# Kernel optimization log

Measured on AMD Instinct MI355X. Metric: run time of the kernel, lower is better.

Reference implementation:

```python
import jax, jax.numpy as jnp
import numpy as np

B, S, D, H = 2, 2048, 1024, 16
HD = D // H


def setup_inputs() -> dict:
    key = jax.random.key(0)
    ks = jax.random.split(key, 6)
    std = 1.0 / np.sqrt(D)
    return {
        "hidden_states": jax.random.normal(ks[0], (B, S, D), dtype=jnp.float32),
        "attention_mask": jnp.zeros((B, 1, S, S), dtype=jnp.float32),
        "Wq": jax.random.normal(ks[1], (D, D), dtype=jnp.float32) * std,
        "bq": jnp.zeros((D,), dtype=jnp.float32),
        "Wk": jax.random.normal(ks[2], (D, D), dtype=jnp.float32) * std,
        "bk": jnp.zeros((D,), dtype=jnp.float32),
        "Wv": jax.random.normal(ks[3], (D, D), dtype=jnp.float32) * std,
        "bv": jnp.zeros((D,), dtype=jnp.float32),
        "Wo": jax.random.normal(ks[4], (D, D), dtype=jnp.float32) * std,
        "bo": jnp.zeros((D,), dtype=jnp.float32),
    }


def reference(hidden_states, attention_mask, Wq, bq, Wk, bk, Wv, bv, Wo, bo):
    scale = HD ** (-0.5)
    # torch Linear: y = x @ W^T + b
    def proj(x, W, b):
        y = jnp.einsum('bsd,ed->bse', x, W) + b
        return y.reshape(B, S, H, HD).transpose(0, 2, 1, 3)  # [B,H,S,HD]
    q = proj(hidden_states, Wq, bq)
    k = proj(hidden_states, Wk, bk)
    v = proj(hidden_states, Wv, bv)
    scores = jnp.einsum('bhqd,bhkd->bhqk', q, k) * scale + attention_mask
    attn = jax.nn.softmax(scores, axis=-1)  # dropout p=0.0 -> identity
    out = jnp.einsum('bhqk,bhkd->bhqd', attn, v)
    out = out.transpose(0, 2, 1, 3).reshape(B, S, D)
    return jnp.einsum('bsd,ed->bse', out, Wo) + bo
```

## Files before the change

kernel.cpp:

```cpp
#include <hip/hip_runtime.h>
#include <hip/hip_bf16.h>
#include <stdint.h>

#define Bb 2
#define Ss 2048
#define Dd 1024
#define Hh 16
#define HD 64

typedef __attribute__((ext_vector_type(8))) __bf16 bf16x8;
typedef __attribute__((ext_vector_type(4))) __bf16 bf16x4;
typedef __attribute__((ext_vector_type(2))) __bf16 bf16x2;
typedef __attribute__((ext_vector_type(4))) float f32x4;
typedef __attribute__((ext_vector_type(16))) float f32x16;

#define LOG2E 1.44269504088896f
#define SCL2 (0.125f * LOG2E)

#define HS_N   (Bb * Ss * Dd)
#define W_N    (Dd * Dd)
#define B_N    (Dd)
#define CAN_HS 0
#define CAN_WQ (CAN_HS + HS_N)
#define CAN_BQ (CAN_WQ + W_N)
#define CAN_WK (CAN_BQ + B_N)
#define CAN_BK (CAN_WK + W_N)
#define CAN_WV (CAN_BK + B_N)
#define CAN_BV (CAN_WV + W_N)
#define CAN_WO (CAN_BV + B_N)
#define CAN_BO (CAN_WO + W_N)
#define CAN_END (CAN_BO + B_N)
#define TSZ    (Bb * Hh * Ss * HD)
#define WS_ELEMS (CAN_END + 4 * TSZ)
#define WS_NEED ((size_t)WS_ELEMS * 2)

__device__ __forceinline__ void gl_lds16(const __bf16* g, __bf16* l) {
  __builtin_amdgcn_global_load_lds(
      (const __attribute__((address_space(1))) void*)g,
      (__attribute__((address_space(3))) void*)l,
      16, 0, 0);
}

__device__ __forceinline__ void cfence() { asm volatile("" ::: "memory"); }

__global__ void canon_kernel(const float* hs, const float* Wq, const float* bq,
                             const float* Wk, const float* bk, const float* Wv,
                             const float* bv, const float* Wo, const float* bo,
                             __bf16* __restrict__ dst) {
  const float* srcs[9] = {hs, Wq, bq, Wk, bk, Wv, bv, Wo, bo};
  const long starts[10] = {CAN_HS, CAN_WQ, CAN_BQ, CAN_WK, CAN_BK,
                           CAN_WV, CAN_BV, CAN_WO, CAN_BO, CAN_END};
  const long nchunks = CAN_END / 8;
  for (long c = blockIdx.x * blockDim.x + threadIdx.x; c < nchunks;
       c += (long)gridDim.x * blockDim.x) {
    const long i = c * 8;
    int seg = 0;
#pragma unroll
    for (int t = 1; t < 9; t++) seg += (i >= starts[t]) ? 1 : 0;
    const float* s = srcs[seg] + (i - starts[seg]);
    bf16x8 v;
#pragma unroll
    for (int e = 0; e < 8; e++) v[e] = (__bf16)s[e];
    *(bf16x8*)(dst + i) = v;
  }
}

template <int MODE, typename OutT>
__global__ __launch_bounds__(256, 2) void gemm_bt(
    const __bf16* __restrict__ A,
    const __bf16* __restrict__ W0, const __bf16* __restrict__ W1,
    const __bf16* __restrict__ W2,
    const __bf16* __restrict__ b0, const __bf16* __restrict__ b1,
    const __bf16* __restrict__ b2,
    OutT* __restrict__ O0, OutT* __restrict__ O1, OutT* __restrict__ O2) {
  __shared__ __align__(16) __bf16 sA[128 * 32];
  __shared__ __align__(16) __bf16 sB[128 * 32];
  const int tid = threadIdx.x;
  const int lane = tid & 63;
  const int wid = tid >> 6;
  const int quad = lane >> 4;
  const int l15 = lane & 15;
  const int mBlock = blockIdx.x * 128;

  const __bf16* W;
  const __bf16* bias;
  OutT* Out;
  int nBlock, which = 0;
  if (MODE == 0) {
    which = blockIdx.y >> 3;
    nBlock = (blockIdx.y & 7) * 128;
    W = which == 0 ? W0 : (which == 1 ? W1 : W2);
    bias = which == 0 ? b0 : (which == 1 ? b1 : b2);
    Out = which == 0 ? O0 : (which == 1 ? O1 : O2);
  } else {
    nBlock = blockIdx.y * 128;
    W = W0;
    bias = b0;
    Out = O0;
  }

  const int waveM = (wid >> 1) * 64;
  const int waveN = (wid & 1) * 64;

  f32x4 acc[4][4] = {};

  const int c1 = wid * 64 + lane;
  const int c2 = c1 + 256;
  const __bf16* Ar1 = A + (mBlock + (c1 >> 2)) * Dd + (c1 & 3) * 8;
  const __bf16* Ar2 = A + (mBlock + (c2 >> 2)) * Dd + (c2 & 3) * 8;
  const __bf16* Wr1 = W + (nBlock + (c1 >> 2)) * Dd + (c1 & 3) * 8;
  const __bf16* Wr2 = W + (nBlock + (c2 >> 2)) * Dd + (c2 & 3) * 8;
  __bf16* ldsA1 = sA + (wid * 64) * 8;
  __bf16* ldsA2 = sA + (wid * 64 + 256) * 8;
  __bf16* ldsB1 = sB + (wid * 64) * 8;
  __bf16* ldsB2 = sB + (wid * 64 + 256) * 8;

  for (int k0 = 0; k0 < Dd; k0 += 32) {
    gl_lds16(Ar1 + k0, ldsA1);
    gl_lds16(Ar2 + k0, ldsA2);
    gl_lds16(Wr1 + k0, ldsB1);
    gl_lds16(Wr2 + k0, ldsB2);
    __syncthreads();

    bf16x8 aF[4], bF[4];
#pragma unroll
    for (int mi = 0; mi < 4; mi++)
      aF[mi] = *(const bf16x8*)(sA + (waveM + mi * 16 + l15) * 32 + quad * 8);
#pragma unroll
    for (int ni = 0; ni < 4; ni++)
      bF[ni] = *(const bf16x8*)(sB + (waveN + ni * 16 + l15) * 32 + quad * 8);
#pragma unroll
    for (int mi = 0; mi < 4; mi++)
#pragma unroll
      for (int ni = 0; ni < 4; ni++)
        acc[mi][ni] = __builtin_amdgcn_mfma_f32_16x16x32_bf16(
            aF[mi], bF[ni], acc[mi][ni], 0, 0, 0);
    __syncthreads();
  }

#pragma unroll
  for (int ni = 0; ni < 4; ni++) {
    const int ng = nBlock + waveN + ni * 16 + l15;
    const float bv = (float)bias[ng];
#pragma unroll
    for (int mi = 0; mi < 4; mi++) {
      const int mg0 = mBlock + waveM + mi * 16 + quad * 4;
      if (MODE == 0 && which == 2) {
        const int b = mg0 >> 11, s0 = mg0 & 2047;
        const int h = ng >> 6, hd = ng & 63;
        bf16x4 pk;
#pragma unroll
        for (int r = 0; r < 4; r++) pk[r] = (__bf16)(acc[mi][ni][r] + bv);
        *(bf16x4*)((__bf16*)Out + (((b * Hh + h) * HD + hd) * Ss) + s0) = pk;
      } else {
#pragma unroll
        for (int r = 0; r < 4; r++) {
          float v = acc[mi][ni][r] + bv;
          const int m = mg0 + r;
          if (MODE == 0) {
            if (which == 0) v *= SCL2;
            const int b = m >> 11, s = m & 2047;
            const int h = ng >> 6, hd = ng & 63;
            Out[(((b * Hh + h) * Ss + s) * HD) + hd] = (OutT)v;
          } else {
            Out[m * Dd + ng] = (OutT)v;
          }
        }
      }
    }
  }
}

__global__ __launch_bounds__(256, 4) void attn_fused(
    const __bf16* __restrict__ Qg, const __bf16* __restrict__ Kg,
    const __bf16* __restrict__ Vt, const float* __restrict__ Mf,
    __bf16* __restrict__ Og) {
  __shared__ __align__(16) union {
    __bf16 buf[2][8192];
    struct {
      float O[2][64][32];
      float L[2][32];
    } m;
  } sh;

  const int tid = threadIdx.x;
  const int lane = tid & 63;
  const int wid = tid >> 6;
  const int qg = wid & 1;
  const int kvh = wid >> 1;
  const int l31 = lane & 31;
  const int hi = lane >> 5;
  const int bh = blockIdx.y;
  const int b = bh >> 4;
  const int h = bh & 15;
  const int qw = blockIdx.x * 64 + qg * 32 + l31;

  const __bf16* Qp = Qg + (size_t)bh * Ss * HD;
  const __bf16* Kp = Kg + (size_t)bh * Ss * HD;
  const __bf16* Vp = Vt + (size_t)bh * HD * Ss;
  const float* Mrow = Mf + ((size_t)b * Ss + qw) * Ss + 32 * kvh + 4 * hi;

  bf16x8 qf[4];
#pragma unroll
  for (int k = 0; k < 4; k++)
    qf[k] = *(const bf16x8*)(Qp + (size_t)qw * HD + k * 16 + hi * 8);

  const int cA = tid, cB = 256 + tid;
#define STAGE_KV(BI, KVS)                                                     \
  {                                                                           \
    __bf16* kb = sh.buf[BI];                                                  \
    gl_lds16(Kp + ((KVS) + ((cA & 255) >> 2)) * HD + (cA >> 8) * 32 +         \
                 (cA & 3) * 8, kb + cA * 8);                                  \
    gl_lds16(Kp + ((KVS) + ((cB & 255) >> 2)) * HD + (cB >> 8) * 32 +         \
                 (cB & 3) * 8, kb + cB * 8);                                  \
    __bf16* vb = sh.buf[BI] + 4096;                                           \
    gl_lds16(Vp + (size_t)((cA & 255) >> 2) * Ss + (KVS) + (cA >> 8) * 32 +   \
                 (cA & 3) * 8, vb + cA * 8);                                  \
    gl_lds16(Vp + (size_t)((cB & 255) >> 2) * Ss + (KVS) + (cB >> 8) * 32 +   \
                 (cB & 3) * 8, vb + cB * 8);                                  \
  }

  f32x16 o[2] = {};
  f32x4 lacc = {0.f, 0.f, 0.f, 0.f};

  STAGE_KV(0, 0);

  for (int it = 0; it < 32; ++it) {
    const int kv0 = it * 64;
    const int bufc = it & 1;
    cfence();
    __builtin_amdgcn_s_barrier();
    cfence();
    f32x4 mc[4];
#pragma unroll
    for (int g = 0; g < 4; g++) mc[g] = *(const f32x4*)(Mrow + kv0 + g * 8);
    cfence();
    if (it < 31) {
      STAGE_KV(bufc ^ 1, kv0 + 64);
      cfence();
      asm volatile("s_waitcnt vmcnt(8)" ::: "memory");
    } else {
      asm volatile("s_waitcnt vmcnt(4)" ::: "memory");
    }
    __builtin_amdgcn_s_barrier();
    cfence();

    f32x16 sacc = {};
#pragma unroll
    for (int k = 0; k < 4; k++) {
      bf16x8 kf = *(const bf16x8*)(sh.buf[bufc] +
                                   ((k >> 1) * 64 + kvh * 32 + l31) * 32 +
                                   (k & 1) * 16 + hi * 8);
      sacc = __builtin_amdgcn_mfma_f32_32x32x16_bf16(kf, qf[k], sacc, 0, 0, 0);
    }

    f32x4 sv[4];
#pragma unroll
    for (int g = 0; g < 4; g++)
#pragma unroll
      for (int r = 0; r < 4; r++)
        sv[g][r] = __builtin_amdgcn_exp2f(sacc[g * 4 + r] + mc[g][r] * LOG2E);
    lacc += (sv[0] + sv[1]) + (sv[2] + sv[3]);

    bf16x4 pk[4];
#pragma unroll
    for (int g = 0; g < 4; g++)
#pragma unroll
      for (int r = 0; r < 4; r++) pk[g][r] = (__bf16)sv[g][r];
    union pu { bf16x4 v; uint32_t w[2]; };
    pu s0, s1, r0, r1;
    s0.v = hi ? pk[0] : pk[1];
    s1.v = hi ? pk[2] : pk[3];
    r0.w[0] = __shfl_xor((int)s0.w[0], 32);
    r0.w[1] = __shfl_xor((int)s0.w[1], 32);
    r1.w[0] = __shfl_xor((int)s1.w[0], 32);
    r1.w[1] = __shfl_xor((int)s1.w[1], 32);
    bf16x8 pf[2];
    {
      bf16x4 lo0 = hi ? r0.v : pk[0], hi0 = hi ? pk[1] : r0.v;
      bf16x4 lo1 = hi ? r1.v : pk[2], hi1 = hi ? pk[3] : r1.v;
#pragma unroll
      for (int e = 0; e < 4; e++) {
        pf[0][e] = lo0[e]; pf[0][e + 4] = hi0[e];
        pf[1][e] = lo1[e]; pf[1][e + 4] = hi1[e];
      }
    }

#pragma unroll
    for (int k = 0; k < 2; k++)
#pragma unroll
      for (int hb = 0; hb < 2; hb++) {
        bf16x8 vf = *(const bf16x8*)(sh.buf[bufc] + 4096 +
                                     (kvh * 64 + hb * 32 + l31) * 32 +
                                     k * 16 + hi * 8);
        o[hb] = __builtin_amdgcn_mfma_f32_32x32x16_bf16(vf, pf[k], o[hb],
                                                        0, 0, 0);
      }
  }

  float l = lacc[0] + lacc[1] + lacc[2] + lacc[3];
  l += __shfl_xor(l, 32);

  __syncthreads();
  if (kvh == 1) {
#pragma unroll
    for (int hb = 0; hb < 2; hb++)
#pragma unroll
      for (int r = 0; r < 16; r++) {
        const int hd = hb * 32 + (r & 3) + 8 * (r >> 2) + 4 * hi;
        sh.m.O[qg][hd][l31] = o[hb][r];
      }
    if (hi == 0) sh.m.L[qg][l31] = l;
  }
  __syncthreads();
  if (kvh == 0) {
#pragma unroll
    for (int hb = 0; hb < 2; hb++)
#pragma unroll
      for (int r = 0; r < 16; r++) {
        const int hd = hb * 32 + (r & 3) + 8 * (r >> 2) + 4 * hi;
        o[hb][r] += sh.m.O[qg][hd][l31];
      }
    l += sh.m.L[qg][l31];
    const float inv = 1.0f / l;
    __bf16* Ow = Og + (((size_t)b * Ss + qw) * Hh + h) * HD;
#pragma unroll
    for (int hb = 0; hb < 2; hb++)
#pragma unroll
      for (int g = 0; g < 4; g++) {
        const int hd = hb * 32 + g * 8 + 4 * hi;
        bf16x2 w0, w1;
        w0[0] = (__bf16)(o[hb][g * 4 + 0] * inv);
        w0[1] = (__bf16)(o[hb][g * 4 + 1] * inv);
        w1[0] = (__bf16)(o[hb][g * 4 + 2] * inv);
        w1[1] = (__bf16)(o[hb][g * 4 + 3] * inv);
        *(bf16x2*)(Ow + hd) = w0;
        *(bf16x2*)(Ow + hd + 2) = w1;
      }
  }
}

extern "C" void kernel_launch(void* const* d_in, const int* in_sizes, int n_in,
                              void* d_out, int out_size, void* d_ws,
                              size_t ws_size, hipStream_t stream) {
  if (ws_size < WS_NEED) return;

  __bf16* ws = (__bf16*)d_ws;
  const __bf16* hsC = ws + CAN_HS;
  const __bf16* WqC = ws + CAN_WQ;
  const __bf16* bqC = ws + CAN_BQ;
  const __bf16* WkC = ws + CAN_WK;
  const __bf16* bkC = ws + CAN_BK;
  const __bf16* WvC = ws + CAN_WV;
  const __bf16* bvC = ws + CAN_BV;
  const __bf16* WoC = ws + CAN_WO;
  const __bf16* boC = ws + CAN_BO;
  __bf16* Q = ws + CAN_END;
  __bf16* K = Q + TSZ;
  __bf16* V = K + TSZ;
  __bf16* AW = V + TSZ;
  float* out = (float*)d_out;

  canon_kernel<<<2048, 256, 0, stream>>>(
      (const float*)d_in[0], (const float*)d_in[2], (const float*)d_in[3],
      (const float*)d_in[4], (const float*)d_in[5], (const float*)d_in[6],
      (const float*)d_in[7], (const float*)d_in[8], (const float*)d_in[9], ws);
  gemm_bt<0, __bf16><<<dim3(32, 24), 256, 0, stream>>>(
      hsC, WqC, WkC, WvC, bqC, bkC, bvC, Q, K, V);
  attn_fused<<<dim3(32, 32), 256, 0, stream>>>(Q, K, V, (const float*)d_in[1],
                                               AW);
  gemm_bt<1, float><<<dim3(32, 8), 256, 0, stream>>>(
      AW, WoC, WoC, WoC, boC, boC, boC, out, out, out);
}
```

Before: 256.0 us.

## Split output GEMM into narrower-tile kernel and relayout attention K/V LDS tiles

The templated GEMM is split into a QKV-projection kernel and a dedicated output-projection kernel. The output kernel uses 128x64 tiles with K-step 64, which doubles the grid to 512 blocks for better CU coverage and halves barrier count per K. Separately, the attention kernel's K/V shared-memory staging is relaid out into 16-element-wide sub-tiles, with matching fragment read addresses, likely to reduce LDS bank conflicts. The trade-off is more redundant A-tile loads in the output GEMM and more duplicated code.

```diff
diff --git a/kernel.cpp b/kernel.cpp
--- a/kernel.cpp
+++ b/kernel.cpp
@@ -65,14 +65,13 @@
   }
 }
 
-template <int MODE, typename OutT>
-__global__ __launch_bounds__(256, 2) void gemm_bt(
+__global__ __launch_bounds__(256, 2) void gemm_qkv(
     const __bf16* __restrict__ A,
     const __bf16* __restrict__ W0, const __bf16* __restrict__ W1,
     const __bf16* __restrict__ W2,
     const __bf16* __restrict__ b0, const __bf16* __restrict__ b1,
     const __bf16* __restrict__ b2,
-    OutT* __restrict__ O0, OutT* __restrict__ O1, OutT* __restrict__ O2) {
+    __bf16* __restrict__ O0, __bf16* __restrict__ O1, __bf16* __restrict__ O2) {
   __shared__ __align__(16) __bf16 sA[128 * 32];
   __shared__ __align__(16) __bf16 sB[128 * 32];
   const int tid = threadIdx.x;
@@ -82,22 +81,11 @@
   const int l15 = lane & 15;
   const int mBlock = blockIdx.x * 128;
 
-  const __bf16* W;
-  const __bf16* bias;
-  OutT* Out;
-  int nBlock, which = 0;
-  if (MODE == 0) {
-    which = blockIdx.y >> 3;
-    nBlock = (blockIdx.y & 7) * 128;
-    W = which == 0 ? W0 : (which == 1 ? W1 : W2);
-    bias = which == 0 ? b0 : (which == 1 ? b1 : b2);
-    Out = which == 0 ? O0 : (which == 1 ? O1 : O2);
-  } else {
-    nBlock = blockIdx.y * 128;
-    W = W0;
-    bias = b0;
-    Out = O0;
-  }
+  const int which = blockIdx.y >> 3;
+  const int nBlock = (blockIdx.y & 7) * 128;
+  const __bf16* W = which == 0 ? W0 : (which == 1 ? W1 : W2);
+  const __bf16* bias = which == 0 ? b0 : (which == 1 ? b1 : b2);
+  __bf16* Out = which == 0 ? O0 : (which == 1 ? O1 : O2);
 
   const int waveM = (wid >> 1) * 64;
   const int waveN = (wid & 1) * 64;
@@ -110,10 +98,10 @@
   const __bf16* Ar2 = A + (mBlock + (c2 >> 2)) * Dd + (c2 & 3) * 8;
   const __bf16* Wr1 = W + (nBlock + (c1 >> 2)) * Dd + (c1 & 3) * 8;
   const __bf16* Wr2 = W + (nBlock + (c2 >> 2)) * Dd + (c2 & 3) * 8;
-  __bf16* ldsA1 = sA + (wid * 64) * 8;
-  __bf16* ldsA2 = sA + (wid * 64 + 256) * 8;
-  __bf16* ldsB1 = sB + (wid * 64) * 8;
-  __bf16* ldsB2 = sB + (wid * 64 + 256) * 8;
+  __bf16* ldsA1 = sA + c1 * 8;
+  __bf16* ldsA2 = sA + c2 * 8;
+  __bf16* ldsB1 = sB + c1 * 8;
+  __bf16* ldsB2 = sB + c2 * 8;
 
   for (int k0 = 0; k0 < Dd; k0 += 32) {
     gl_lds16(Ar1 + k0, ldsA1);
@@ -145,28 +133,92 @@
 #pragma unroll
     for (int mi = 0; mi < 4; mi++) {
       const int mg0 = mBlock + waveM + mi * 16 + quad * 4;
-      if (MODE == 0 && which == 2) {
+      if (which == 2) {
         const int b = mg0 >> 11, s0 = mg0 & 2047;
         const int h = ng >> 6, hd = ng & 63;
         bf16x4 pk;
 #pragma unroll
         for (int r = 0; r < 4; r++) pk[r] = (__bf16)(acc[mi][ni][r] + bv);
-        *(bf16x4*)((__bf16*)Out + (((b * Hh + h) * HD + hd) * Ss) + s0) = pk;
+        *(bf16x4*)(Out + (((b * Hh + h) * HD + hd) * Ss) + s0) = pk;
       } else {
 #pragma unroll
         for (int r = 0; r < 4; r++) {
           float v = acc[mi][ni][r] + bv;
+          if (which == 0) v *= SCL2;
           const int m = mg0 + r;
-          if (MODE == 0) {
-            if (which == 0) v *= SCL2;
-            const int b = m >> 11, s = m & 2047;
-            const int h = ng >> 6, hd = ng & 63;
-            Out[(((b * Hh + h) * Ss + s) * HD) + hd] = (OutT)v;
-          } else {
-            Out[m * Dd + ng] = (OutT)v;
-          }
+          const int b = m >> 11, s = m & 2047;
+          const int h = ng >> 6, hd = ng & 63;
+          Out[(((b * Hh + h) * Ss + s) * HD) + hd] = (__bf16)v;
         }
       }
+    }
+  }
+}
+
+__global__ __launch_bounds__(256, 2) void gemm_out(
+    const __bf16* __restrict__ A, const __bf16* __restrict__ W,
+    const __bf16* __restrict__ bias, float* __restrict__ Out) {
+  __shared__ __align__(16) __bf16 sA[2][128][32];
+  __shared__ __align__(16) __bf16 sB[2][64][32];
+  const int tid = threadIdx.x;
+  const int lane = tid & 63;
+  const int wid = tid >> 6;
+  const int quad = lane >> 4;
+  const int l15 = lane & 15;
+  const int mBlock = blockIdx.x * 128;
+  const int nBlock = blockIdx.y * 64;
+
+  const int waveM = (wid >> 1) * 64;
+  const int waveN = (wid & 1) * 32;
+
+  f32x4 acc[4][2] = {};
+
+  for (int k0 = 0; k0 < Dd; k0 += 64) {
+#pragma unroll
+    for (int j = 0; j < 4; j++) {
+      const int c = j * 256 + tid;
+      gl_lds16(A + (mBlock + ((c >> 2) & 127)) * Dd + k0 + (c >> 9) * 32 +
+                   (c & 3) * 8,
+               &sA[0][0][0] + c * 8);
+    }
+#pragma unroll
+    for (int j = 0; j < 2; j++) {
+      const int c = j * 256 + tid;
+      gl_lds16(W + (nBlock + ((c >> 2) & 63)) * Dd + k0 + (c >> 8) * 32 +
+                   (c & 3) * 8,
+               &sB[0][0][0] + c * 8);
+    }
+    __syncthreads();
+
+#pragma unroll
+    for (int ks = 0; ks < 2; ks++) {
+      bf16x8 aF[4], bF[2];
+#pragma unroll
+      for (int mi = 0; mi < 4; mi++)
+        aF[mi] = *(const bf16x8*)&sA[ks][waveM + mi * 16 + l15][quad * 8];
+#pragma unroll
+      for (int ni = 0; ni < 2; ni++)
+        bF[ni] = *(const bf16x8*)&sB[ks][waveN + ni * 16 + l15][quad * 8];
+#pragma unroll
+      for (int mi = 0; mi < 4; mi++)
+#pragma unroll
+        for (int ni = 0; ni < 2; ni++)
+          acc[mi][ni] = __builtin_amdgcn_mfma_f32_16x16x32_bf16(
+              aF[mi], bF[ni], acc[mi][ni], 0, 0, 0);
+    }
+    __syncthreads();
+  }
+
+#pragma unroll
+  for (int ni = 0; ni < 2; ni++) {
+    const int ng = nBlock + waveN + ni * 16 + l15;
+    const float bv = (float)bias[ng];
+#pragma unroll
+    for (int mi = 0; mi < 4; mi++) {
+      const int mg0 = mBlock + waveM + mi * 16 + quad * 4;
+#pragma unroll
+      for (int r = 0; r < 4; r++)
+        Out[(mg0 + r) * Dd + ng] = acc[mi][ni][r] + bv;
     }
   }
 }
@@ -209,15 +261,15 @@
 #define STAGE_KV(BI, KVS)                                                     \
   {                                                                           \
     __bf16* kb = sh.buf[BI];                                                  \
-    gl_lds16(Kp + ((KVS) + ((cA & 255) >> 2)) * HD + (cA >> 8) * 32 +         \
-                 (cA & 3) * 8, kb + cA * 8);                                  \
-    gl_lds16(Kp + ((KVS) + ((cB & 255) >> 2)) * HD + (cB >> 8) * 32 +         \
-                 (cB & 3) * 8, kb + cB * 8);                                  \
+    gl_lds16(Kp + ((KVS) + ((cA >> 1) & 63)) * HD + (cA >> 7) * 16 +          \
+                 (cA & 1) * 8, kb + cA * 8);                                  \
+    gl_lds16(Kp + ((KVS) + ((cB >> 1) & 63)) * HD + (cB >> 7) * 16 +          \
+                 (cB & 1) * 8, kb + cB * 8);                                  \
     __bf16* vb = sh.buf[BI] + 4096;                                           \
-    gl_lds16(Vp + (size_t)((cA & 255) >> 2) * Ss + (KVS) + (cA >> 8) * 32 +   \
-                 (cA & 3) * 8, vb + cA * 8);                                  \
-    gl_lds16(Vp + (size_t)((cB & 255) >> 2) * Ss + (KVS) + (cB >> 8) * 32 +   \
-                 (cB & 3) * 8, vb + cB * 8);                                  \
+    gl_lds16(Vp + (size_t)((cA >> 1) & 63) * Ss + (KVS) + (cA >> 7) * 16 +    \
+                 (cA & 1) * 8, vb + cA * 8);                                  \
+    gl_lds16(Vp + (size_t)((cB >> 1) & 63) * Ss + (KVS) + (cB >> 7) * 16 +    \
+                 (cB & 1) * 8, vb + cB * 8);                                  \
   }
 
   f32x16 o[2] = {};
@@ -248,9 +300,8 @@
     f32x16 sacc = {};
 #pragma unroll
     for (int k = 0; k < 4; k++) {
-      bf16x8 kf = *(const bf16x8*)(sh.buf[bufc] +
-                                   ((k >> 1) * 64 + kvh * 32 + l31) * 32 +
-                                   (k & 1) * 16 + hi * 8);
+      bf16x8 kf = *(const bf16x8*)(sh.buf[bufc] + k * 1024 +
+                                   (kvh * 32 + l31) * 16 + hi * 8);
       sacc = __builtin_amdgcn_mfma_f32_32x32x16_bf16(kf, qf[k], sacc, 0, 0, 0);
     }
 
@@ -291,8 +342,8 @@
 #pragma unroll
       for (int hb = 0; hb < 2; hb++) {
         bf16x8 vf = *(const bf16x8*)(sh.buf[bufc] + 4096 +
-                                     (kvh * 64 + hb * 32 + l31) * 32 +
-                                     k * 16 + hi * 8);
+                                     (kvh * 2 + k) * 1024 +
+                                     (hb * 32 + l31) * 16 + hi * 8);
         o[hb] = __builtin_amdgcn_mfma_f32_32x32x16_bf16(vf, pf[k], o[hb],
                                                         0, 0, 0);
       }
@@ -365,10 +416,9 @@
       (const float*)d_in[0], (const float*)d_in[2], (const float*)d_in[3],
       (const float*)d_in[4], (const float*)d_in[5], (const float*)d_in[6],
       (const float*)d_in[7], (const float*)d_in[8], (const float*)d_in[9], ws);
-  gemm_bt<0, __bf16><<<dim3(32, 24), 256, 0, stream>>>(
-      hsC, WqC, WkC, WvC, bqC, bkC, bvC, Q, K, V);
+  gemm_qkv<<<dim3(32, 24), 256, 0, stream>>>(hsC, WqC, WkC, WvC, bqC, bkC,
+                                             bvC, Q, K, V);
   attn_fused<<<dim3(32, 32), 256, 0, stream>>>(Q, K, V, (const float*)d_in[1],
                                                AW);
-  gemm_bt<1, float><<<dim3(32, 8), 256, 0, stream>>>(
-      AW, WoC, WoC, WoC, boC, boC, boC, out, out, out);
-}
+  gemm_out<<<dim3(32, 16), 256, 0, stream>>>(AW, WoC, boC, out);
+}
```

Result: slower. 261.4 us (+2.1%).
